# Optimization experiments

Measured on AMD Instinct MI355X. Metric: run time of the kernel, lower is better.

## Reference

```python
import jax, jax.numpy as jnp
import numpy as np

NFFT = 512
NFILT = 40
EPS = float(np.finfo(np.float64).eps)  # np.finfo(float).eps in the original


def _mel_fbank(fs: int, nfft: int = NFFT, nfilt: int = NFILT) -> np.ndarray:
    # Faithful reconstruction of the original triangular filterbank,
    # including int() truncation of bin edges and the (j+1) offsets.
    high_freq_mel = 2595.0 * np.log10(1.0 + fs / 2.0 / 700.0)
    mel_points = np.linspace(0.0, high_freq_mel, nfilt + 2)
    hz_points = 700.0 * (10.0 ** (mel_points / 2595.0) - 1.0)
    b = hz_points / (fs / 2.0) * (nfft / 2.0)
    fbank = np.zeros((nfilt, nfft // 2 + 1), dtype=np.float64)
    for i in range(1, nfilt + 1):
        left, center, right = int(b[i - 1]), int(b[i]), int(b[i + 1])
        for j in range(left, center):
            fbank[i - 1, j + 1] = (j + 1 - b[i - 1]) / (b[i] - b[i - 1])
        for j in range(center, right):
            fbank[i - 1, j + 1] = (b[i + 1] - (j + 1)) / (b[i + 1] - b[i])
    return fbank.astype(np.float32)


def setup_inputs() -> dict:
    key = jax.random.key(0)
    Signals = jax.random.normal(key, (32, 50000), dtype=jnp.float32)
    return {"Signals": Signals, "fs": 1000}


def reference(Signals, fs):
    # NOTE: in the original, Signal = Signals[i].unsqueeze(0) makes the
    # pre-emphasis slice arithmetic operate on an empty array, so the
    # "emphasized" signal is just the raw signal. The hamming window is
    # computed but never applied. Both bugs replicated faithfully.
    B, L = Signals.shape
    frame_length = int(round(0.025 * fs))   # 25
    frame_step = int(round(0.01 * fs))      # 10
    num_frames = int(np.ceil(abs(L - frame_length) / frame_step)) + 1
    pad_len = (num_frames - 1) * frame_step + frame_length

    padded = jnp.pad(Signals, ((0, 0), (0, pad_len - L)))  # [B, pad_len]
    # static frame-gather indices [num_frames, frame_length]
    idx = (np.arange(frame_length)[None, :]
           + np.arange(0, num_frames * frame_step, frame_step)[:, None])
    frames = padded[:, idx]                                # [B, T, frame_length]

    mag = jnp.abs(jnp.fft.rfft(frames, NFFT))              # [B, T, NFFT//2+1]
    pow_frames = mag * mag * (1.0 / NFFT)

    fbank = jnp.asarray(_mel_fbank(fs))                    # [nfilt, NFFT//2+1]
    fb = jnp.einsum('btf,nf->btn', pow_frames, fbank)      # [B, T, nfilt]
    fb = jnp.where(fb == 0, EPS, fb)
    return (20.0 * jnp.log10(fb)).astype(jnp.float32)
```

## Files before the change

kernel.cpp:

```cpp
#include <hip/hip_runtime.h>

#define NFILT   40
#define FLEN    25
#define FSTEP   10
#define BATCH   32
#define SIGLEN  50000
#define NFRAMES 4999
#define EPSV    2.220446049250313e-16f
#define TPB     128
#define NBLK    40
#define SPAN4   1296
#define OSTR    41

namespace ctab {

constexpr double PI   = 3.14159265358979323846264338327950288;
constexpr double LN10 = 2.30258509299404568401799145468436421;

constexpr double cln(double y) {
    double z = (y - 1.0) / (y + 1.0);
    double z2 = z * z, term = z, s = 0.0;
    for (int k = 0; k < 40; ++k) { s += term / (2.0 * k + 1.0); term *= z2; }
    return 2.0 * s;
}
constexpr double cexp(double x) {
    double s = 1.0, term = 1.0;
    for (int i = 1; i <= 24; ++i) { term *= x / (double)i; s += term; }
    return s;
}
constexpr double ccospi_r(double t) {
    double x = PI * t, x2 = x * x;
    double s = 1.0, term = 1.0;
    for (int k = 1; k <= 16; ++k) { term *= -x2 / ((2.0 * k - 1.0) * (2.0 * k)); s += term; }
    return s;
}
constexpr double ccospi_m(int m) {
    int mm = m & 511;
    if (mm > 256) mm = 512 - mm;
    if (mm <= 128) return ccospi_r(mm / 256.0);
    return -ccospi_r((256 - mm) / 256.0);
}

struct CTab {
    float c[NFILT][FLEN];
    constexpr CTab() : c{} {
        double ct[512] = {};
        for (int m = 0; m < 512; ++m) ct[m] = ccospi_m(m);
        double fs = 1000.0;
        double high_mel = 2595.0 * (cln(1.0 + fs / 2.0 / 700.0) / LN10);
        double b[NFILT + 2] = {};
        for (int i = 0; i < NFILT + 2; ++i) {
            double mel = high_mel * (double)i / (double)(NFILT + 1);
            double hz  = 700.0 * (cexp(mel / 2595.0 * LN10) - 1.0);
            b[i] = hz / (fs / 2.0) * 256.0;
        }
        for (int f = 0; f < NFILT; ++f) {
            int left = (int)b[f], center = (int)b[f + 1], right = (int)b[f + 2];
            for (int d = 0; d < FLEN; ++d) {
                double acc = 0.0;
                for (int j = left; j < right; ++j) {
                    double w = (j < center)
                        ? ((double)(j + 1) - b[f])     / (b[f + 1] - b[f])
                        : (b[f + 2] - (double)(j + 1)) / (b[f + 2] - b[f + 1]);
                    acc += w * ct[((j + 1) * d) & 511];
                }
                double v = acc / 512.0;
                if (d) v *= 2.0;
                c[f][d] = (float)v;
            }
        }
    }
};
static constexpr CTab CT{};

}

__global__ __launch_bounds__(TPB, 3) void mel_main(const float* __restrict__ sig,
                                                   float* __restrict__ out) {
    const int b   = blockIdx.y;
    const int t0  = blockIdx.x * TPB;
    const int tid = threadIdx.x;

    __shared__ float s_sig[SPAN4];
    __shared__ float s_stage[TPB * OSTR];

    const int base = t0 * FSTEP;
    const int rem  = SIGLEN - base;
    const float* sb = sig + (size_t)b * SIGLEN + base;
    #pragma unroll
    for (int i = tid * 4; i < SPAN4; i += TPB * 4) {
        float4 v = make_float4(0.f, 0.f, 0.f, 0.f);
        if (i + 4 <= rem) {
            v = *reinterpret_cast<const float4*>(sb + i);
        } else if (i < rem) {
            v.x = sb[i];
            if (i + 1 < rem) v.y = sb[i + 1];
            if (i + 2 < rem) v.z = sb[i + 2];
        }
        *reinterpret_cast<float4*>(s_sig + i) = v;
    }
    __syncthreads();

    float x[FLEN];
    const float* sp = s_sig + tid * FSTEP;
    #pragma unroll
    for (int n = 0; n < FLEN; ++n) x[n] = sp[n];

    float R[FLEN];
    #pragma unroll
    for (int d = 0; d < FLEN; ++d) {
        float a = 0.f;
        #pragma unroll
        for (int n = 0; n + d < FLEN; ++n) a = fmaf(x[n], x[n + d], a);
        R[d] = a;
    }

    float* st = s_stage + tid * OSTR;
    #pragma unroll
    for (int f = 0; f < NFILT; ++f) {
        float a = 0.f;
        #pragma unroll
        for (int d = 0; d < FLEN; ++d)
            a = fmaf(ctab::CT.c[f][d], R[d], a);
        if (a < EPSV) a = EPSV;
        st[f] = 6.0205999132796239f * __log2f(a);
    }
    __syncthreads();

    const size_t outbase = ((size_t)b * NFRAMES + t0) * NFILT;
    #pragma unroll
    for (int j = 0; j < 10; ++j) {
        int i4 = j * TPB + tid;
        int fr = i4 / 10;
        int fl = i4 - fr * 10;
        if (t0 + fr < NFRAMES) {
            const float* q = s_stage + fr * OSTR + fl * 4;
            float4 v = make_float4(q[0], q[1], q[2], q[3]);
            *reinterpret_cast<float4*>(out + outbase + (size_t)i4 * 4) = v;
        }
    }
}

extern "C" void kernel_launch(void* const* d_in, const int* in_sizes, int n_in,
                              void* d_out, int out_size, void* d_ws, size_t ws_size,
                              hipStream_t stream) {
    const float* sig = (const float*)d_in[0];
    float* out = (float*)d_out;
    dim3 grid(NBLK, BATCH);
    mel_main<<<grid, dim3(TPB), 0, stream>>>(sig, out);
}
```

Before: 18.26 us.

## Load frames directly from global into registers with one-wave blocks

Removes the shared-memory signal staging and its barrier; each thread now reads its own 25-sample frame straight from global memory as float2 loads, with the last frame zero-padded by hand. Blocks shrink to 64 threads (one wavefront), grid grows to 79x32, and launch bounds rise to 4. The aim is to cut shared-memory traffic and sync overhead and to spread the work over more blocks on the many CUs. In exchange, overlapping frames are fetched redundantly from global memory (about 2.5x the bytes, mostly caught by L1/L2) through strided per-thread loads.

```diff
diff --git a/kernel.cpp b/kernel.cpp
--- a/kernel.cpp
+++ b/kernel.cpp
@@ -7,9 +7,8 @@
 #define SIGLEN  50000
 #define NFRAMES 4999
 #define EPSV    2.220446049250313e-16f
-#define TPB     128
-#define NBLK    40
-#define SPAN4   1296
+#define TPB     64
+#define NBLKX   79
 #define OSTR    41
 
 namespace ctab {
@@ -75,36 +74,37 @@
 
 }
 
-__global__ __launch_bounds__(TPB, 3) void mel_main(const float* __restrict__ sig,
+__global__ __launch_bounds__(TPB, 4) void mel_main(const float* __restrict__ sig,
                                                    float* __restrict__ out) {
-    const int b   = blockIdx.y;
-    const int t0  = blockIdx.x * TPB;
-    const int tid = threadIdx.x;
+    const int b    = blockIdx.y;
+    const int t0   = blockIdx.x * TPB;
+    const int lane = threadIdx.x;
+    const int t    = t0 + lane;
 
-    __shared__ float s_sig[SPAN4];
     __shared__ float s_stage[TPB * OSTR];
 
-    const int base = t0 * FSTEP;
-    const int rem  = SIGLEN - base;
-    const float* sb = sig + (size_t)b * SIGLEN + base;
-    #pragma unroll
-    for (int i = tid * 4; i < SPAN4; i += TPB * 4) {
-        float4 v = make_float4(0.f, 0.f, 0.f, 0.f);
-        if (i + 4 <= rem) {
-            v = *reinterpret_cast<const float4*>(sb + i);
-        } else if (i < rem) {
-            v.x = sb[i];
-            if (i + 1 < rem) v.y = sb[i + 1];
-            if (i + 2 < rem) v.z = sb[i + 2];
+    float x[FLEN];
+    if (t < NFRAMES - 1) {
+        const float* gp = sig + (size_t)b * SIGLEN + t * FSTEP;
+        #pragma unroll
+        for (int q = 0; q < 12; ++q) {
+            float2 v = *reinterpret_cast<const float2*>(gp + q * 2);
+            x[q * 2] = v.x; x[q * 2 + 1] = v.y;
         }
-        *reinterpret_cast<float4*>(s_sig + i) = v;
+        x[24] = gp[24];
+    } else if (t == NFRAMES - 1) {
+        const float* gp = sig + (size_t)b * SIGLEN + t * FSTEP;
+        #pragma unroll
+        for (int q = 0; q < 10; ++q) {
+            float2 v = *reinterpret_cast<const float2*>(gp + q * 2);
+            x[q * 2] = v.x; x[q * 2 + 1] = v.y;
+        }
+        #pragma unroll
+        for (int n = 20; n < FLEN; ++n) x[n] = 0.f;
+    } else {
+        #pragma unroll
+        for (int n = 0; n < FLEN; ++n) x[n] = 0.f;
     }
-    __syncthreads();
-
-    float x[FLEN];
-    const float* sp = s_sig + tid * FSTEP;
-    #pragma unroll
-    for (int n = 0; n < FLEN; ++n) x[n] = sp[n];
 
     float R[FLEN];
     #pragma unroll
@@ -115,7 +115,7 @@
         R[d] = a;
     }
 
-    float* st = s_stage + tid * OSTR;
+    float* st = s_stage + lane * OSTR;
     #pragma unroll
     for (int f = 0; f < NFILT; ++f) {
         float a = 0.f;
@@ -130,7 +130,7 @@
     const size_t outbase = ((size_t)b * NFRAMES + t0) * NFILT;
     #pragma unroll
     for (int j = 0; j < 10; ++j) {
-        int i4 = j * TPB + tid;
+        int i4 = j * TPB + lane;
         int fr = i4 / 10;
         int fl = i4 - fr * 10;
         if (t0 + fr < NFRAMES) {
@@ -146,6 +146,6 @@
                               hipStream_t stream) {
     const float* sig = (const float*)d_in[0];
     float* out = (float*)d_out;
-    dim3 grid(NBLK, BATCH);
+    dim3 grid(NBLKX, BATCH);
     mel_main<<<grid, dim3(TPB), 0, stream>>>(sig, out);
 }
```

After: 17.62 us. 1.04x faster.
